# Performance work log

Hardware: AMD Instinct MI355X
Metric: run time of the kernel (lower is better)

Reference implementation:

```python
import math
import jax, jax.numpy as jnp
import numpy as np

W_SIZE = 7
NUM_HEADS = 12


def _shift_masks(w: int, d: int):
    # upper/lower mask (applied to last row of windows)
    ul = np.zeros((w * w, w * w), np.float32)
    ul[-d * w:, :-d * w] = -np.inf
    ul[:-d * w, -d * w:] = -np.inf
    # left/right mask (applied to last column of windows)
    lr = np.zeros((w, w, w, w), np.float32)
    lr[:, -d:, :, :-d] = -np.inf
    lr[:, :-d, :, -d:] = -np.inf
    lr = lr.reshape(w * w, w * w)
    return jnp.asarray(ul), jnp.asarray(lr)


def _rel_pos_index(w: int):
    # standard Swin relative-position index, shape (w*w, w*w), values in [0, (2w-1)^2)
    coords = np.stack(np.meshgrid(np.arange(w), np.arange(w), indexing='ij'), 0).reshape(2, -1)  # (2, w*w)
    rel = coords[:, :, None] - coords[:, None, :]  # (2, ww, ww)
    idx = (rel[0] + w - 1) * (2 * w - 1) + (rel[1] + w - 1)
    return jnp.asarray(idx, dtype=jnp.int32)


def setup_inputs() -> dict:
    key = jax.random.key(0)
    ks = jax.random.split(key, 6)
    E, w = 384, W_SIZE
    return {
        'x': jax.random.normal(ks[0], (32, 56, 56, E), jnp.float32),
        'w_qkv': jax.random.normal(ks[1], (3 * E, E), jnp.float32) * 0.02,
        'b_qkv': jax.random.normal(ks[2], (3 * E,), jnp.float32) * 0.02,
        'w_proj': jax.random.normal(ks[3], (E, E), jnp.float32) * 0.02,
        'b_proj': jax.random.normal(ks[4], (E,), jnp.float32) * 0.02,
        'rel_table': jax.random.normal(ks[5], ((2 * w - 1) ** 2, NUM_HEADS), jnp.float32) * 0.02,
    }


def reference(x, w_qkv, b_qkv, w_proj, b_proj, rel_table):
    w = W_SIZE
    heads = NUM_HEADS
    B, H, Wd, C = x.shape
    hd = C // heads
    nh, nw, ww = H // w, Wd // w, w * w

    # shift (matches torch roll(shifts=(-w//2, -w//2)) == -4 for w=7)
    x = jnp.roll(x, ((-w) // 2, (-w) // 2), axis=(1, 2))

    # window partition: (B, nh, nw, ww, C)
    xw = x.reshape(B, nh, w, nw, w, C).transpose(0, 1, 3, 2, 4, 5).reshape(B, nh, nw, ww, C)

    qkv = xw @ w_qkv.T + b_qkv  # (B, nh, nw, ww, 3C)
    q, k, v = jnp.split(qkv, 3, axis=-1)

    def heads_first(t):  # (B, nh, nw, heads, ww, hd)
        return t.reshape(B, nh, nw, ww, heads, hd).transpose(0, 1, 2, 4, 3, 5)

    q, k, v = heads_first(q), heads_first(k), heads_first(v)

    attn = jnp.einsum('bhwnqd,bhwnkd->bhwnqk', q, k) * (1.0 / math.sqrt(hd))

    # relative position bias: (heads, ww, ww)
    bias = rel_table[_rel_pos_index(w)].transpose(2, 0, 1)
    attn = attn + bias

    # shift masks on last row / last column of windows
    ul, lr = _shift_masks(w, w // 2)
    mask = jnp.zeros((nh, nw, 1, ww, ww), attn.dtype)
    mask = mask.at[-1].add(ul)
    mask = mask.at[:, -1].add(lr)
    attn = attn + mask

    p = jax.nn.softmax(attn, axis=-1)
    o = jnp.einsum('bhwnqk,bhwnkd->bhwnqd', p, v)  # (B, nh, nw, heads, ww, hd)

    # merge heads and un-window
    o = o.transpose(0, 1, 2, 4, 3, 5).reshape(B, nh, nw, w, w, C)
    o = o.transpose(0, 1, 3, 2, 4, 5).reshape(B, H, Wd, C)

    o = jnp.roll(o, (w // 2, w // 2), axis=(1, 2))
    return o @ w_proj.T + b_proj
```

## Files before the change

kernel.cpp:

```cpp
#include <hip/hip_runtime.h>
#include <hip/hip_bf16.h>


typedef __bf16 bf16x8 __attribute__((ext_vector_type(8)));
typedef float  floatx4 __attribute__((ext_vector_type(4)));
typedef short  short8  __attribute__((ext_vector_type(8)));

#define MFMA16(a, b, c) __builtin_amdgcn_mfma_f32_16x16x32_bf16((a), (b), (c), 0, 0, 0)

static __device__ __forceinline__ void gload_lds16(const void* g, void* l) {
  __builtin_amdgcn_global_load_lds(
      (const __attribute__((address_space(1))) void*)g,
      (__attribute__((address_space(3))) void*)l, 16, 0, 0);
}

static __device__ __forceinline__ int src_off(int gm) {
  int win = gm / 49, t = gm - win * 49;
  int b = win >> 6, rr = win & 63;
  int wi = rr >> 3, wj = rr & 7;
  int ty = t / 7, tx = t - ty * 7;
  int y = wi * 7 + ty + 4; if (y >= 56) y -= 56;
  int x = wj * 7 + tx + 4; if (x >= 56) x -= 56;
  return ((b * 56 + y) * 56 + x) * 384;
}

static __device__ __forceinline__ int dst_off(int gm) {
  int win = gm / 49, t = gm - win * 49;
  int b = win >> 6, rr = win & 63;
  int wi = rr >> 3, wj = rr & 7;
  int ty = t / 7, tx = t - ty * 7;
  int y = wi * 7 + ty + 3; if (y >= 56) y -= 56;
  int x = wj * 7 + tx + 3; if (x >= 56) x -= 56;
  return ((b * 56 + y) * 56 + x) * 384;
}

static __device__ __forceinline__ float bf_lo(unsigned u) {
  union { unsigned v; float f; } c; c.v = u << 16; return c.f;
}
static __device__ __forceinline__ float bf_hi(unsigned u) {
  union { unsigned v; float f; } c; c.v = u & 0xFFFF0000u; return c.f;
}

__global__ __launch_bounds__(256) void prep_kernel(
    const float* __restrict__ w_qkv, const float* __restrict__ w_proj,
    const float* __restrict__ rel_table,
    __hip_bfloat16* __restrict__ wqkv_bf, __hip_bfloat16* __restrict__ wproj_bf,
    __hip_bfloat16* __restrict__ bias2) {
  const int N1 = 3 * 384 * 384;
  const int N2 = 384 * 384;
  const int N3 = 12 * 4 * 4 * 64 * 4;
  int i = blockIdx.x * 256 + threadIdx.x;
  if (i < N1) wqkv_bf[i] = __float2bfloat16(w_qkv[i]);
  int j = i - N1;
  if (j >= 0 && j < N2) wproj_bf[j] = __float2bfloat16(w_proj[j]);
  int k = i - N1 - N2;
  if (k >= 0 && k < N3) {
    int r = k & 3;
    int lp = (k >> 2) & 63;
    int ni = (k >> 8) & 3;
    int mi = (k >> 10) & 3;
    int head = k >> 12;
    int m = mi * 16 + (lp & 15);
    int n = ni * 16 + (lp >> 4) * 4 + r;
    float val = 0.f;
    if (m < 49 && n < 49) {
      int dy = m / 7 - n / 7 + 6;
      int dx = m % 7 - n % 7 + 6;
      val = rel_table[(dy * 13 + dx) * 12 + head];
    }
    bias2[k] = __float2bfloat16(val);
  }
}

__global__ __launch_bounds__(256) void xconv_kernel(
    const float* __restrict__ x, __hip_bfloat16* __restrict__ xw) {
  int gid = blockIdx.x * 256 + threadIdx.x;
  int row = gid / 48;
  int c = (gid - row * 48) * 8;
  int so = src_off(row) + c;
  floatx4 a = *(const floatx4*)(x + so);
  floatx4 b = *(const floatx4*)(x + so + 4);
  union { __hip_bfloat16 h[8]; short8 s; } u;
#pragma unroll
  for (int i = 0; i < 4; ++i) {
    u.h[i]     = __float2bfloat16(a[i]);
    u.h[4 + i] = __float2bfloat16(b[i]);
  }
  *(short8*)(xw + (size_t)row * 384 + c) = u.s;
}

__global__ __launch_bounds__(256) void qkv_kernel(
    const __hip_bfloat16* __restrict__ xw, const __hip_bfloat16* __restrict__ wq,
    const float* __restrict__ bqkv,
    __hip_bfloat16* __restrict__ qb, __hip_bfloat16* __restrict__ kb,
    __hip_bfloat16* __restrict__ vt) {
  __shared__ __hip_bfloat16 lds[2 * 16384];
  int blk = blockIdx.x;
  int b2 = (blk & 7) * 882 + (blk >> 3);
  int mt = b2 / 9, nt = b2 - mt * 9;
  int tid = threadIdx.x;
  int l = tid & 63, wv = tid >> 6;
  int wm = wv >> 1, wn = wv & 1;
  int g = l >> 4, q16 = l & 15;

  const bool swapped = (nt >= 6);
  const int aro = (swapped ? wn : wm) * 64;
  const int bro = (swapped ? wm : wn) * 64;

  int sr = tid >> 3;
  int sc = tid & 7;
  int scs = sc ^ (sr & 7);

  const __hip_bfloat16* abase = xw + (size_t)(mt * 128) * 384;
  const __hip_bfloat16* bbase = wq + (size_t)(nt * 128) * 384;

  floatx4 acc[4][4];
#pragma unroll
  for (int i = 0; i < 4; ++i)
#pragma unroll
    for (int j = 0; j < 4; ++j)
#pragma unroll
      for (int r = 0; r < 4; ++r) acc[i][j][r] = 0.f;

  auto stage = [&](int buf, int kt) {
    int k0 = kt * 64;
    __hip_bfloat16* la = lds + buf * 16384;
#pragma unroll
    for (int c = 0; c < 4; ++c) {
      int r = c * 32 + sr;
      gload_lds16(abase + (size_t)r * 384 + k0 + scs * 8, la + c * 2048 + tid * 8);
      gload_lds16(bbase + (size_t)r * 384 + k0 + scs * 8, la + 8192 + c * 2048 + tid * 8);
    }
  };

  auto compute = [&](int buf) {
    const __hip_bfloat16* la = lds + buf * 16384;
    const __hip_bfloat16* lb = la + 8192;
#pragma unroll
    for (int kk = 0; kk < 2; ++kk) {
      bf16x8 af[4], bf[4];
#pragma unroll
      for (int i = 0; i < 4; ++i) {
        int r = aro + i * 16 + q16;
        int cp = (kk * 4 + g) ^ (r & 7);
        af[i] = *(const bf16x8*)(la + r * 64 + cp * 8);
      }
#pragma unroll
      for (int i = 0; i < 4; ++i) {
        int r = bro + i * 16 + q16;
        int cp = (kk * 4 + g) ^ (r & 7);
        bf[i] = *(const bf16x8*)(lb + r * 64 + cp * 8);
      }
      if (!swapped) {
#pragma unroll
        for (int i = 0; i < 4; ++i)
#pragma unroll
          for (int j = 0; j < 4; ++j)
            acc[i][j] = MFMA16(af[i], bf[j], acc[i][j]);
      } else {
#pragma unroll
        for (int i = 0; i < 4; ++i)
#pragma unroll
          for (int j = 0; j < 4; ++j)
            acc[i][j] = MFMA16(bf[i], af[j], acc[i][j]);
      }
    }
  };

  stage(0, 0);
  stage(1, 1);
#pragma unroll
  for (int t = 0; t < 6; ++t) {
    if (t < 5) asm volatile("s_waitcnt vmcnt(8)" ::: "memory");
    else       asm volatile("s_waitcnt vmcnt(0)" ::: "memory");
    __builtin_amdgcn_s_barrier();
    __builtin_amdgcn_sched_barrier(0);
    compute(t & 1);
    if (t < 4) {
      __builtin_amdgcn_s_barrier();
      stage(t & 1, t + 2);
    }
  }

  if (!swapped) {
    const bool isq = (nt < 3);
    __hip_bfloat16* ob2 = isq ? qb : kb;
#pragma unroll
    for (int ni = 0; ni < 4; ++ni) {
      int n = nt * 128 + wn * 64 + ni * 16 + q16;
      float bn = bqkv[n];
      int nn = isq ? n : (n - 384);
#pragma unroll
      for (int mi = 0; mi < 4; ++mi) {
#pragma unroll
        for (int r = 0; r < 4; ++r) {
          int gm = mt * 128 + wm * 64 + mi * 16 + g * 4 + r;
          float v = acc[mi][ni][r] + bn;
          if (isq) v *= 0.17677669529663687f;
          ob2[gm * 384 + nn] = __float2bfloat16(v);
        }
      }
    }
  } else {
    int win4[4], t4[4];
#pragma unroll
    for (int bj = 0; bj < 4; ++bj) {
      int gm = mt * 128 + wn * 64 + bj * 16 + q16;
      int w = gm / 49;
      win4[bj] = w;
      t4[bj] = gm - w * 49;
    }
#pragma unroll
    for (int ai = 0; ai < 4; ++ai) {
#pragma unroll
      for (int r = 0; r < 4; ++r) {
        int n = nt * 128 + wm * 64 + ai * 16 + g * 4 + r;
        float bn = bqkv[n];
        int nnv = n - 768;
#pragma unroll
        for (int bj = 0; bj < 4; ++bj) {
          vt[((size_t)win4[bj] * 384 + nnv) * 64 + t4[bj]] =
              __float2bfloat16(acc[ai][bj][r] + bn);
        }
      }
    }
  }
}

__global__ __launch_bounds__(256, 3) void attnproj_kernel(
    const __hip_bfloat16* __restrict__ qb, const __hip_bfloat16* __restrict__ kb,
    const __hip_bfloat16* __restrict__ vt, const __hip_bfloat16* __restrict__ bias2,
    const __hip_bfloat16* __restrict__ wp, const float* __restrict__ bproj,
    float* __restrict__ out) {
  __shared__ __hip_bfloat16 o_lds[49][392];
  __shared__ __hip_bfloat16 p_lds[4][16][72];
  int blk = blockIdx.x;
  int win = (blk & 7) * 256 + (blk >> 3);
  int tid = threadIdx.x;
  int wv = tid >> 6, l = tid & 63;
  int g = l >> 4, q16 = l & 15;
  int wr = win & 63;
  const bool lastrow = ((wr >> 3) == 7);
  const bool lastcol = ((wr & 7) == 7);

  unsigned long long badbits = 0ull;
#pragma unroll
  for (int mi = 0; mi < 4; ++mi) {
    int m = mi * 16 + q16;
    int m7 = m % 7;
    bool m28 = (m >= 28), m74 = (m7 >= 4);
#pragma unroll
    for (int ni = 0; ni < 4; ++ni) {
#pragma unroll
      for (int r = 0; r < 4; ++r) {
        int n = ni * 16 + g * 4 + r;
        bool bad = (n >= 49) ||
                   (lastrow && (m28 != (n >= 28))) ||
                   (lastcol && (m74 != ((n % 7) >= 4)));
        if (bad) badbits |= (1ull << (mi * 16 + ni * 4 + r));
      }
    }
  }

  bf16x8 zf;
#pragma unroll
  for (int i = 0; i < 8; ++i) zf[i] = (__bf16)0.0f;
  floatx4 zc;
  zc[0] = zc[1] = zc[2] = zc[3] = 0.f;

#pragma unroll 1
  for (int hh = 0; hh < 3; ++hh) {
    int head = wv * 3 + hh;
    const __hip_bfloat16* qp = qb + (size_t)(win * 49) * 384 + head * 32 + g * 8;
    const __hip_bfloat16* kp = kb + (size_t)(win * 49) * 384 + head * 32 + g * 8;

    bf16x8 aq[4], bk[4];
#pragma unroll
    for (int mi = 0; mi < 4; ++mi) {
      int row = mi * 16 + q16;
      if (row < 49) {
        aq[mi] = *(const bf16x8*)(qp + row * 384);
        bk[mi] = *(const bf16x8*)(kp + row * 384);
      } else {
        aq[mi] = zf;
        bk[mi] = zf;
      }
    }

    floatx4 st[4][4];
    __builtin_amdgcn_s_setprio(1);
#pragma unroll
    for (int ni = 0; ni < 4; ++ni)
#pragma unroll
      for (int mi = 0; mi < 4; ++mi)
        st[ni][mi] = MFMA16(bk[ni], aq[mi], zc);
    __builtin_amdgcn_s_setprio(0);

    const __hip_bfloat16* vp = vt + ((size_t)win * 384 + head * 32) * 64;
    bf16x8 bv[2][2];
#pragma unroll
    for (int ks = 0; ks < 2; ++ks)
#pragma unroll
      for (int n2 = 0; n2 < 2; ++n2)
        bv[ks][n2] = *(const bf16x8*)(vp + (n2 * 16 + q16) * 64 + ks * 32 + g * 8);

    const __hip_bfloat16* b2 = bias2 + (size_t)head * 4096;

#pragma unroll
    for (int mi = 0; mi < 4; ++mi) {
      uint2 braw[4];
#pragma unroll
      for (int ni = 0; ni < 4; ++ni)
        braw[ni] = *(const uint2*)(b2 + ((mi * 4 + ni) * 64 + l) * 4);

      float vals[4][4];
      float mx = -1e30f;
#pragma unroll
      for (int ni = 0; ni < 4; ++ni) {
#pragma unroll
        for (int r = 0; r < 4; ++r) {
          float bb = (r == 0) ? bf_lo(braw[ni].x) : (r == 1) ? bf_hi(braw[ni].x)
                     : (r == 2) ? bf_lo(braw[ni].y) : bf_hi(braw[ni].y);
          bool bad = (badbits >> (mi * 16 + ni * 4 + r)) & 1;
          float v = bad ? -1e30f : (st[ni][mi][r] + bb);
          vals[ni][r] = v;
          mx = fmaxf(mx, v);
        }
      }
      mx = fmaxf(mx, __shfl_xor(mx, 16));
      mx = fmaxf(mx, __shfl_xor(mx, 32));
      float sum = 0.f;
#pragma unroll
      for (int ni = 0; ni < 4; ++ni) {
#pragma unroll
        for (int r = 0; r < 4; ++r) {
          float p = __expf(vals[ni][r] - mx);
          vals[ni][r] = p;
          sum += p;
        }
      }
      sum += __shfl_xor(sum, 16);
      sum += __shfl_xor(sum, 32);
      float inv = 1.0f / sum;

#pragma unroll
      for (int ni = 0; ni < 4; ++ni) {
        union { __hip_bfloat16 h[4]; unsigned long long u; } pk;
#pragma unroll
        for (int r = 0; r < 4; ++r) pk.h[r] = __float2bfloat16(vals[ni][r] * inv);
        *(unsigned long long*)&p_lds[wv][q16][ni * 16 + g * 4] = pk.u;
      }

      bf16x8 av0 = *(const bf16x8*)&p_lds[wv][q16][g * 8];
      bf16x8 av1 = *(const bf16x8*)&p_lds[wv][q16][32 + g * 8];
      floatx4 o2[2];
      o2[0] = o2[1] = zc;
#pragma unroll
      for (int n2 = 0; n2 < 2; ++n2) {
        o2[n2] = MFMA16(av0, bv[0][n2], o2[n2]);
        o2[n2] = MFMA16(av1, bv[1][n2], o2[n2]);
      }
#pragma unroll
      for (int r = 0; r < 4; ++r) {
        int m = mi * 16 + g * 4 + r;
        if (m < 49) {
#pragma unroll
          for (int n2 = 0; n2 < 2; ++n2)
            o_lds[m][head * 32 + n2 * 16 + q16] = __float2bfloat16(o2[n2][r]);
        }
      }
    }
  }

  __syncthreads();

  floatx4 pacc[4][6];
#pragma unroll
  for (int i = 0; i < 4; ++i)
#pragma unroll
    for (int j = 0; j < 6; ++j)
#pragma unroll
      for (int r = 0; r < 4; ++r) pacc[i][j][r] = 0.f;

  for (int k0 = 0; k0 < 384; k0 += 32) {
    bf16x8 af[4], bfr[6];
#pragma unroll
    for (int mi = 0; mi < 4; ++mi) {
      int row = mi * 16 + q16;
      row = row < 49 ? row : 48;
      af[mi] = *(const bf16x8*)&o_lds[row][k0 + g * 8];
    }
#pragma unroll
    for (int ni = 0; ni < 6; ++ni) {
      int brow = wv * 96 + ni * 16 + q16;
      bfr[ni] = *(const bf16x8*)(wp + (size_t)brow * 384 + k0 + g * 8);
    }
    __builtin_amdgcn_s_setprio(1);
#pragma unroll
    for (int mi = 0; mi < 4; ++mi)
#pragma unroll
      for (int ni = 0; ni < 6; ++ni)
        pacc[mi][ni] = MFMA16(af[mi], bfr[ni], pacc[mi][ni]);
    __builtin_amdgcn_s_setprio(0);
  }

#pragma unroll
  for (int mi = 0; mi < 4; ++mi) {
#pragma unroll
    for (int r = 0; r < 4; ++r) {
      int m = mi * 16 + g * 4 + r;
      if (m < 49) {
        int off = dst_off(win * 49 + m);
#pragma unroll
        for (int ni = 0; ni < 6; ++ni) {
          int n = wv * 96 + ni * 16 + q16;
          out[off + n] = pacc[mi][ni][r] + bproj[n];
        }
      }
    }
  }
}

extern "C" void kernel_launch(void* const* d_in, const int* in_sizes, int n_in,
                              void* d_out, int out_size, void* d_ws, size_t ws_size,
                              hipStream_t stream) {
  const float* x         = (const float*)d_in[0];
  const float* w_qkv     = (const float*)d_in[1];
  const float* b_qkv     = (const float*)d_in[2];
  const float* w_proj    = (const float*)d_in[3];
  const float* b_proj    = (const float*)d_in[4];
  const float* rel_table = (const float*)d_in[5];
  float* out = (float*)d_out;

  char* ws = (char*)d_ws;
  const size_t OFF_WQKV  = 0;
  const size_t OFF_WPROJ = 884736;
  const size_t OFF_BIAS2 = 1179648;
  const size_t OFF_Q     = 1572864;
  const size_t OFF_K     = OFF_Q + 77070336;
  const size_t OFF_VT    = OFF_K + 77070336;

  __hip_bfloat16* wqkv_bf  = (__hip_bfloat16*)(ws + OFF_WQKV);
  __hip_bfloat16* wproj_bf = (__hip_bfloat16*)(ws + OFF_WPROJ);
  __hip_bfloat16* bias2    = (__hip_bfloat16*)(ws + OFF_BIAS2);
  __hip_bfloat16* qb       = (__hip_bfloat16*)(ws + OFF_Q);
  __hip_bfloat16* kb       = (__hip_bfloat16*)(ws + OFF_K);
  __hip_bfloat16* vt       = (__hip_bfloat16*)(ws + OFF_VT);
  __hip_bfloat16* xw       = (__hip_bfloat16*)d_out;


  prep_kernel<<<3072, 256, 0, stream>>>(w_qkv, w_proj, rel_table, wqkv_bf, wproj_bf, bias2);
  xconv_kernel<<<18816, 256, 0, stream>>>(x, xw);
  qkv_kernel<<<7056, 256, 0, stream>>>(xw, wqkv_bf, b_qkv, qb, kb, vt);
  attnproj_kernel<<<2048, 256, 0, stream>>>(qb, kb, vt, bias2, wproj_bf, b_proj, out);
}
```

Baseline: 406.3 us.

## Cut register pressure in attnproj: per-row scores, shuffle P transpose, split projection

The attention-projection kernel now computes QK^T one query tile at a time and feeds P to the PV MFMA through register shuffles instead of a per-wave LDS staging buffer. The projection runs as two passes of 48 output columns, which halves the accumulator registers. Padding columns are masked by baking -1e30 into the bias table, so mask bits only need computing for last-row and last-column windows. The launch bounds go from 3 to 4 blocks per SM for higher occupancy. In exchange there are more shuffles and select instructions, and the projection re-reads o_lds in the second pass.

```diff
diff --git a/kernel.cpp b/kernel.cpp
--- a/kernel.cpp
+++ b/kernel.cpp
@@ -5,6 +5,7 @@
 typedef __bf16 bf16x8 __attribute__((ext_vector_type(8)));
 typedef float  floatx4 __attribute__((ext_vector_type(4)));
 typedef short  short8  __attribute__((ext_vector_type(8)));
+typedef unsigned long long u64;
 
 #define MFMA16(a, b, c) __builtin_amdgcn_mfma_f32_16x16x32_bf16((a), (b), (c), 0, 0, 0)
 
@@ -62,7 +63,7 @@
     int head = k >> 12;
     int m = mi * 16 + (lp & 15);
     int n = ni * 16 + (lp >> 4) * 4 + r;
-    float val = 0.f;
+    float val = -1e30f;
     if (m < 49 && n < 49) {
       int dy = m / 7 - n / 7 + 6;
       int dx = m % 7 - n % 7 + 6;
@@ -227,13 +228,12 @@
   }
 }
 
-__global__ __launch_bounds__(256, 3) void attnproj_kernel(
+__global__ __launch_bounds__(256, 4) void attnproj_kernel(
     const __hip_bfloat16* __restrict__ qb, const __hip_bfloat16* __restrict__ kb,
     const __hip_bfloat16* __restrict__ vt, const __hip_bfloat16* __restrict__ bias2,
     const __hip_bfloat16* __restrict__ wp, const float* __restrict__ bproj,
     float* __restrict__ out) {
   __shared__ __hip_bfloat16 o_lds[49][392];
-  __shared__ __hip_bfloat16 p_lds[4][16][72];
   int blk = blockIdx.x;
   int win = (blk & 7) * 256 + (blk >> 3);
   int tid = threadIdx.x;
@@ -244,27 +244,25 @@
   const bool lastcol = ((wr & 7) == 7);
 
   unsigned long long badbits = 0ull;
-#pragma unroll
-  for (int mi = 0; mi < 4; ++mi) {
-    int m = mi * 16 + q16;
-    int m7 = m % 7;
-    bool m28 = (m >= 28), m74 = (m7 >= 4);
-#pragma unroll
-    for (int ni = 0; ni < 4; ++ni) {
-#pragma unroll
-      for (int r = 0; r < 4; ++r) {
-        int n = ni * 16 + g * 4 + r;
-        bool bad = (n >= 49) ||
-                   (lastrow && (m28 != (n >= 28))) ||
-                   (lastcol && (m74 != ((n % 7) >= 4)));
-        if (bad) badbits |= (1ull << (mi * 16 + ni * 4 + r));
-      }
-    }
-  }
-
-  bf16x8 zf;
-#pragma unroll
-  for (int i = 0; i < 8; ++i) zf[i] = (__bf16)0.0f;
+  if (lastrow || lastcol) {
+#pragma unroll
+    for (int mi = 0; mi < 4; ++mi) {
+      int m = mi * 16 + q16;
+      int m7 = m % 7;
+      bool m28 = (m >= 28), m74 = (m7 >= 4);
+#pragma unroll
+      for (int ni = 0; ni < 4; ++ni) {
+#pragma unroll
+        for (int r = 0; r < 4; ++r) {
+          int n = ni * 16 + g * 4 + r;
+          bool bad = (lastrow && (m28 != (n >= 28))) ||
+                     (lastcol && (m74 != ((n % 7) >= 4)));
+          if (bad) badbits |= (1ull << (mi * 16 + ni * 4 + r));
+        }
+      }
+    }
+  }
+
   floatx4 zc;
   zc[0] = zc[1] = zc[2] = zc[3] = 0.f;
 
@@ -274,40 +272,36 @@
     const __hip_bfloat16* qp = qb + (size_t)(win * 49) * 384 + head * 32 + g * 8;
     const __hip_bfloat16* kp = kb + (size_t)(win * 49) * 384 + head * 32 + g * 8;
 
-    bf16x8 aq[4], bk[4];
+    bf16x8 bk[4];
+#pragma unroll
+    for (int ni = 0; ni < 4; ++ni) {
+      int row = ni * 16 + q16;
+      row = row < 49 ? row : 48;
+      bk[ni] = *(const bf16x8*)(kp + row * 384);
+    }
+    const __hip_bfloat16* vp = vt + ((size_t)win * 384 + head * 32) * 64;
+    bf16x8 va[2][2];
+#pragma unroll
+    for (int ai = 0; ai < 2; ++ai)
+#pragma unroll
+      for (int ks = 0; ks < 2; ++ks)
+        va[ai][ks] = *(const bf16x8*)(vp + (ai * 16 + q16) * 64 + ks * 32 + g * 8);
+
+    const __hip_bfloat16* b2 = bias2 + (size_t)head * 4096;
+
 #pragma unroll
     for (int mi = 0; mi < 4; ++mi) {
-      int row = mi * 16 + q16;
-      if (row < 49) {
-        aq[mi] = *(const bf16x8*)(qp + row * 384);
-        bk[mi] = *(const bf16x8*)(kp + row * 384);
-      } else {
-        aq[mi] = zf;
-        bk[mi] = zf;
-      }
-    }
-
-    floatx4 st[4][4];
-    __builtin_amdgcn_s_setprio(1);
-#pragma unroll
-    for (int ni = 0; ni < 4; ++ni)
-#pragma unroll
-      for (int mi = 0; mi < 4; ++mi)
-        st[ni][mi] = MFMA16(bk[ni], aq[mi], zc);
-    __builtin_amdgcn_s_setprio(0);
-
-    const __hip_bfloat16* vp = vt + ((size_t)win * 384 + head * 32) * 64;
-    bf16x8 bv[2][2];
-#pragma unroll
-    for (int ks = 0; ks < 2; ++ks)
-#pragma unroll
-      for (int n2 = 0; n2 < 2; ++n2)
-        bv[ks][n2] = *(const bf16x8*)(vp + (n2 * 16 + q16) * 64 + ks * 32 + g * 8);
-
-    const __hip_bfloat16* b2 = bias2 + (size_t)head * 4096;
-
-#pragma unroll
-    for (int mi = 0; mi < 4; ++mi) {
+      int arow = mi * 16 + q16;
+      arow = arow < 49 ? arow : 48;
+      bf16x8 aqm = *(const bf16x8*)(qp + arow * 384);
+
+      floatx4 stm[4];
+      __builtin_amdgcn_s_setprio(1);
+#pragma unroll
+      for (int ni = 0; ni < 4; ++ni)
+        stm[ni] = MFMA16(bk[ni], aqm, zc);
+      __builtin_amdgcn_s_setprio(0);
+
       uint2 braw[4];
 #pragma unroll
       for (int ni = 0; ni < 4; ++ni)
@@ -321,8 +315,8 @@
         for (int r = 0; r < 4; ++r) {
           float bb = (r == 0) ? bf_lo(braw[ni].x) : (r == 1) ? bf_hi(braw[ni].x)
                      : (r == 2) ? bf_lo(braw[ni].y) : bf_hi(braw[ni].y);
-          bool bad = (badbits >> (mi * 16 + ni * 4 + r)) & 1;
-          float v = bad ? -1e30f : (st[ni][mi][r] + bb);
+          float v = stm[ni][r] + bb;
+          if ((badbits >> (mi * 16 + ni * 4 + r)) & 1) v = -1e30f;
           vals[ni][r] = v;
           mx = fmaxf(mx, v);
         }
@@ -343,78 +337,99 @@
       sum += __shfl_xor(sum, 32);
       float inv = 1.0f / sum;
 
+      u64 pk4[4];
 #pragma unroll
       for (int ni = 0; ni < 4; ++ni) {
-        union { __hip_bfloat16 h[4]; unsigned long long u; } pk;
+        union { __hip_bfloat16 h[4]; u64 u; } pk;
 #pragma unroll
         for (int r = 0; r < 4; ++r) pk.h[r] = __float2bfloat16(vals[ni][r] * inv);
-        *(unsigned long long*)&p_lds[wv][q16][ni * 16 + g * 4] = pk.u;
-      }
-
-      bf16x8 av0 = *(const bf16x8*)&p_lds[wv][q16][g * 8];
-      bf16x8 av1 = *(const bf16x8*)&p_lds[wv][q16][32 + g * 8];
+        pk4[ni] = pk.u;
+      }
+
+      bf16x8 bp[2];
+#pragma unroll
+      for (int ks = 0; ks < 2; ++ks) {
+        u64 A  = pk4[2 * ks];
+        u64 A3 = pk4[2 * ks + 1];
+        u64 B16 = __shfl_xor(A, 16);
+        u64 B32 = __shfl_xor(A, 32);
+        u64 B48 = __shfl_xor(A, 48);
+        u64 C16 = __shfl_xor(A3, 16);
+        u64 C32 = __shfl_xor(A3, 32);
+        u64 C48 = __shfl_xor(A3, 48);
+        u64 lo = (g == 0) ? A : (g == 1) ? B48 : (g == 2) ? C32 : C16;
+        u64 hi = (g == 0) ? B16 : (g == 1) ? B32 : (g == 2) ? C48 : A3;
+        union { u64 w[2]; bf16x8 v; } cb;
+        cb.w[0] = lo; cb.w[1] = hi;
+        bp[ks] = cb.v;
+      }
+
       floatx4 o2[2];
       o2[0] = o2[1] = zc;
-#pragma unroll
-      for (int n2 = 0; n2 < 2; ++n2) {
-        o2[n2] = MFMA16(av0, bv[0][n2], o2[n2]);
-        o2[n2] = MFMA16(av1, bv[1][n2], o2[n2]);
-      }
+      __builtin_amdgcn_s_setprio(1);
+#pragma unroll
+      for (int ai = 0; ai < 2; ++ai)
+#pragma unroll
+        for (int ks = 0; ks < 2; ++ks)
+          o2[ai] = MFMA16(va[ai][ks], bp[ks], o2[ai]);
+      __builtin_amdgcn_s_setprio(0);
+
+      int m = mi * 16 + q16;
+      if (m < 49) {
+#pragma unroll
+        for (int ai = 0; ai < 2; ++ai)
+#pragma unroll
+          for (int r = 0; r < 4; ++r)
+            o_lds[m][head * 32 + ai * 16 + g * 4 + r] = __float2bfloat16(o2[ai][r]);
+      }
+    }
+  }
+
+  __syncthreads();
+
+#pragma unroll 1
+  for (int pass = 0; pass < 2; ++pass) {
+    int n0 = wv * 96 + pass * 48;
+    floatx4 pacc[4][3];
+#pragma unroll
+    for (int i = 0; i < 4; ++i)
+#pragma unroll
+      for (int j = 0; j < 3; ++j) pacc[i][j] = zc;
+
+#pragma unroll
+    for (int kk = 0; kk < 12; ++kk) {
+      int k0 = kk * 32;
+      bf16x8 af[4], bfr[3];
+#pragma unroll
+      for (int mi = 0; mi < 4; ++mi) {
+        int row = mi * 16 + q16;
+        row = row < 49 ? row : 48;
+        af[mi] = *(const bf16x8*)&o_lds[row][k0 + g * 8];
+      }
+#pragma unroll
+      for (int ni = 0; ni < 3; ++ni)
+        bfr[ni] = *(const bf16x8*)(wp + (size_t)(n0 + ni * 16 + q16) * 384 + k0 + g * 8);
+      __builtin_amdgcn_s_setprio(1);
+#pragma unroll
+      for (int mi = 0; mi < 4; ++mi)
+#pragma unroll
+        for (int ni = 0; ni < 3; ++ni)
+          pacc[mi][ni] = MFMA16(af[mi], bfr[ni], pacc[mi][ni]);
+      __builtin_amdgcn_s_setprio(0);
+    }
+
+#pragma unroll
+    for (int mi = 0; mi < 4; ++mi) {
 #pragma unroll
       for (int r = 0; r < 4; ++r) {
         int m = mi * 16 + g * 4 + r;
         if (m < 49) {
-#pragma unroll
-          for (int n2 = 0; n2 < 2; ++n2)
-            o_lds[m][head * 32 + n2 * 16 + q16] = __float2bfloat16(o2[n2][r]);
-        }
-      }
-    }
-  }
-
-  __syncthreads();
-
-  floatx4 pacc[4][6];
-#pragma unroll
-  for (int i = 0; i < 4; ++i)
-#pragma unroll
-    for (int j = 0; j < 6; ++j)
-#pragma unroll
-      for (int r = 0; r < 4; ++r) pacc[i][j][r] = 0.f;
-
-  for (int k0 = 0; k0 < 384; k0 += 32) {
-    bf16x8 af[4], bfr[6];
-#pragma unroll
-    for (int mi = 0; mi < 4; ++mi) {
-      int row = mi * 16 + q16;
-      row = row < 49 ? row : 48;
-      af[mi] = *(const bf16x8*)&o_lds[row][k0 + g * 8];
-    }
-#pragma unroll
-    for (int ni = 0; ni < 6; ++ni) {
-      int brow = wv * 96 + ni * 16 + q16;
-      bfr[ni] = *(const bf16x8*)(wp + (size_t)brow * 384 + k0 + g * 8);
-    }
-    __builtin_amdgcn_s_setprio(1);
-#pragma unroll
-    for (int mi = 0; mi < 4; ++mi)
-#pragma unroll
-      for (int ni = 0; ni < 6; ++ni)
-        pacc[mi][ni] = MFMA16(af[mi], bfr[ni], pacc[mi][ni]);
-    __builtin_amdgcn_s_setprio(0);
-  }
-
-#pragma unroll
-  for (int mi = 0; mi < 4; ++mi) {
-#pragma unroll
-    for (int r = 0; r < 4; ++r) {
-      int m = mi * 16 + g * 4 + r;
-      if (m < 49) {
-        int off = dst_off(win * 49 + m);
-#pragma unroll
-        for (int ni = 0; ni < 6; ++ni) {
-          int n = wv * 96 + ni * 16 + q16;
-          out[off + n] = pacc[mi][ni][r] + bproj[n];
+          int off = dst_off(win * 49 + m);
+#pragma unroll
+          for (int ni = 0; ni < 3; ++ni) {
+            int n = n0 + ni * 16 + q16;
+            out[off + n] = pacc[mi][ni][r] + bproj[n];
+          }
         }
       }
     }
```

Measured after the change: 379.1 us. 6.7% less time.
